# Optimization experiments

Measured on AMD Instinct MI355X. Metric: run time of the kernel, lower is better.

The kernel has to match this reference:

```python
import jax, jax.numpy as jnp
import numpy as np

# --- model constants (from init_kwargs) ---
COUNT = 8          # number of layer stacks (king buckets)
L1 = 3072          # input feature dim (2*L1//2 == L1)
L2 = 15            # first hidden dim per stack (l1 outputs L2+1: L2 hidden + 1 skip)
L3 = 32            # second hidden dim per stack
SQ_CORR = 127.0 / 128.0   # sqcrele_correction_factor
MAX_ACT = 1.0             # max_hidden_activation (clipped ReLU ceiling)
BATCH = 32768


def setup_inputs() -> dict:
    key = jax.random.key(0)
    ks = jax.random.split(key, 8)
    x = jax.random.normal(ks[0], (BATCH, L1), dtype=jnp.float32)
    routing_data = jax.random.randint(ks[1], (BATCH,), 0, COUNT, dtype=jnp.int64)
    # StackedLinear weights: [count, out_features, in_features]
    w1 = jax.random.normal(ks[2], (COUNT, L2 + 1, L1), dtype=jnp.float32) * 0.01
    b1 = jax.random.normal(ks[3], (COUNT, L2 + 1), dtype=jnp.float32) * 0.01
    w2 = jax.random.normal(ks[4], (COUNT, L3, 2 * L2), dtype=jnp.float32) * 0.05
    b2 = jax.random.normal(ks[5], (COUNT, L3), dtype=jnp.float32) * 0.01
    w3 = jax.random.normal(ks[6], (COUNT, 1, L3), dtype=jnp.float32) * 0.05
    b3 = jnp.zeros((COUNT, 1), dtype=jnp.float32)  # output bias zeroed in __init__
    return {"x": x, "routing_data": routing_data,
            "w1": w1, "b1": b1, "w2": w2, "b2": b2, "w3": w3, "b3": b3}


def reference(x, routing_data, w1, b1, w2, b2, w3, b3):
    # l1: apply all COUNT linears to the shared input -> [B, count, L2+1]
    l1c = jnp.einsum('bi,coi->bco', x, w1) + b1
    l1x, l1x_out = l1c[..., :L2], l1c[..., L2:]            # [B,c,L2], [B,c,1]
    sqr_l1x = (l1x * l1x) * SQ_CORR
    h1 = jnp.clip(jnp.concatenate([sqr_l1x, l1x], axis=2), 0.0, MAX_ACT)  # [B,c,2*L2]
    # l2: per-stack linear -> [B, count, L3]
    h2 = jnp.clip(jnp.einsum('bci,coi->bco', h1, w2) + b2, 0.0, MAX_ACT)
    # output: per-stack linear -> [B, count, 1], plus skip connection
    l3x = jnp.einsum('bci,coi->bco', h2, w3) + b3 + l1x_out
    # hard-index routing: gather the selected stack per batch element -> [B, 1]
    idx = routing_data.astype(jnp.int32)[:, None, None]
    return jnp.take_along_axis(l3x, idx, axis=1).squeeze(1)
```

## Files before the change

### kernel.cpp

```cpp
#include <hip/hip_runtime.h>

#define NEXP   8
#define L1DIM  3072
#define BATCH  32768
#define SQCORR (127.0f / 128.0f)
#define CHUNK  256
#define NCHUNK (L1DIM / CHUNK)

#define CUR_STRIDE  16
#define WS_CURSORS  0
#define WS_SORTED   (NEXP * CUR_STRIDE)
#define NBLK_SORT   (BATCH / 256)
#define BLK_PER_E   (BATCH / 16)
#define NBLK_MAIN   (NEXP * BLK_PER_E)

__global__ void init_k(int* ws) {
    if (threadIdx.x < NEXP)
        ws[WS_CURSORS + threadIdx.x * CUR_STRIDE] = threadIdx.x * BATCH;
}

__global__ void scatter_k(const int* __restrict__ routing, int* ws) {
    __shared__ int h[NEXP];
    __shared__ int base[NEXP];
    if (threadIdx.x < NEXP) h[threadIdx.x] = 0;
    __syncthreads();
    int i = blockIdx.x * 256 + threadIdx.x;
    int e = routing[i];
    int rank = atomicAdd(&h[e], 1);
    __syncthreads();
    if (threadIdx.x < NEXP)
        base[threadIdx.x] =
            atomicAdd(&ws[WS_CURSORS + threadIdx.x * CUR_STRIDE], h[threadIdx.x]);
    __syncthreads();
    ws[WS_SORTED + base[e] + rank] = i;
}

__device__ __forceinline__ void lds_cp16(void* lds, const void* g) {
    __builtin_amdgcn_global_load_lds(
        (const __attribute__((address_space(1))) void*)g,
        (__attribute__((address_space(3))) void*)lds, 16, 0, 0);
}

__global__ __launch_bounds__(256, 3) void moe_main_k(
        const float* __restrict__ x, const int* __restrict__ ws,
        const float* __restrict__ w1, const float* __restrict__ b1,
        const float* __restrict__ w2, const float* __restrict__ b2,
        const float* __restrict__ w3, const float* __restrict__ b3,
        float* __restrict__ out) {
    __shared__ float xs[3][16][CHUNK];
    __shared__ float tot[4][64];

    const int e   = blockIdx.x % NEXP;
    const int b16 = (blockIdx.x / NEXP) * 16;
    const int n   = ws[WS_CURSORS + e * CUR_STRIDE] - e * BATCH;
    if (b16 >= n) return;

    const int tid  = threadIdx.x;
    const int wid  = tid >> 6;
    const int lane = tid & 63;
    const int r0   = wid * 4;
    const int loff = lane * 4;

    int rows[4];
    const float* xp[4];
    #pragma unroll
    for (int q = 0; q < 4; ++q) {
        int s = b16 + r0 + q;
        rows[q] = (s < n) ? ws[WS_SORTED + e * BATCH + s] : -1;
        int r = rows[q] < 0 ? 0 : rows[q];
        xp[q] = x + (size_t)r * L1DIM;
    }
    const float* w1e = w1 + (size_t)e * 16 * L1DIM;

    auto issue_x = [&](int t, int b) {
        const int koff = t * CHUNK + loff;
        #pragma unroll
        for (int q = 0; q < 4; ++q)
            lds_cp16(&xs[b][r0 + q][loff], xp[q] + koff);
    };

    float acc[64];
    #pragma unroll
    for (int k = 0; k < 64; ++k) acc[k] = 0.0f;

    issue_x(0, 0);
    issue_x(1, 1);

    #pragma unroll 1
    for (int t = 0; t < NCHUNK; ++t) {
        const int xb = t % 3;
        asm volatile("s_waitcnt vmcnt(4)" ::: "memory");

        float4 xv[4];
        #pragma unroll
        for (int q = 0; q < 4; ++q)
            xv[q] = *(const float4*)&xs[xb][r0 + q][loff];

        const float* wc = w1e + t * CHUNK + loff;
        float4 wv[16];
        #pragma unroll
        for (int o = 0; o < 16; ++o)
            wv[o] = *(const float4*)(wc + (size_t)o * L1DIM);

        __builtin_amdgcn_sched_barrier(0);
        if (t + 2 < NCHUNK) issue_x(t + 2, (t + 2) % 3);
        __builtin_amdgcn_sched_barrier(0);

        #pragma unroll
        for (int o = 0; o < 16; ++o) {
            #pragma unroll
            for (int q = 0; q < 4; ++q) {
                float s = acc[q * 16 + o];
                s = fmaf(xv[q].x, wv[o].x, s);
                s = fmaf(xv[q].y, wv[o].y, s);
                s = fmaf(xv[q].z, wv[o].z, s);
                s = fmaf(xv[q].w, wv[o].w, s);
                acc[q * 16 + o] = s;
            }
        }
    }

    #pragma unroll
    for (int s = 0; s < 6; ++s) {
        const int mask = 32 >> s;
        const bool hi = (lane & mask) != 0;
        #pragma unroll
        for (int k = 0; k < 32; ++k) {
            if (k >= mask) break;
            float give = hi ? acc[k] : acc[k + mask];
            float got  = __shfl_xor(give, mask, 64);
            float keep = hi ? acc[k + mask] : acc[k];
            acc[k] = keep + got;
        }
    }

    tot[wid][lane] = acc[0];
    __syncthreads();

    const int q = lane >> 4;
    const int j = lane & 15;
    const int row = rows[q];

    const float* tq = &tot[wid][q * 16];
    float l1x_out = tq[15] + b1[e * 16 + 15];

    float h1v[30];
    #pragma unroll
    for (int i = 0; i < 15; ++i) {
        float t = tq[i] + b1[e * 16 + i];
        float sq = t * t * SQCORR;
        h1v[i]      = fminf(fmaxf(sq, 0.0f), 1.0f);
        h1v[i + 15] = fminf(fmaxf(t,  0.0f), 1.0f);
    }

    float s0 = b2[e * 32 + j];
    float s1 = b2[e * 32 + 16 + j];
    const float* w2e = w2 + (size_t)e * 32 * 30;
    #pragma unroll
    for (int i = 0; i < 30; ++i) {
        s0 = fmaf(h1v[i], w2e[j * 30 + i], s0);
        s1 = fmaf(h1v[i], w2e[(16 + j) * 30 + i], s1);
    }
    s0 = fminf(fmaxf(s0, 0.0f), 1.0f);
    s1 = fminf(fmaxf(s1, 0.0f), 1.0f);

    float p = s0 * w3[e * 32 + j] + s1 * w3[e * 32 + 16 + j];
    #pragma unroll
    for (int m = 8; m >= 1; m >>= 1) p += __shfl_xor(p, m, 64);

    if (j == 0 && row >= 0) out[row] = p + b3[e] + l1x_out;
}

extern "C" void kernel_launch(void* const* d_in, const int* in_sizes, int n_in,
                              void* d_out, int out_size, void* d_ws, size_t ws_size,
                              hipStream_t stream) {
    const float* x       = (const float*)d_in[0];
    const int*   routing = (const int*)d_in[1];
    const float* w1      = (const float*)d_in[2];
    const float* b1      = (const float*)d_in[3];
    const float* w2      = (const float*)d_in[4];
    const float* b2      = (const float*)d_in[5];
    const float* w3      = (const float*)d_in[6];
    const float* b3      = (const float*)d_in[7];
    float* out = (float*)d_out;
    int*   ws  = (int*)d_ws;

    init_k<<<1, 64, 0, stream>>>(ws);
    scatter_k<<<NBLK_SORT, 256, 0, stream>>>(routing, ws);
    moe_main_k<<<NBLK_MAIN, 256, 0, stream>>>(x, ws, w1, b1, w2, b2, w3, b3, out);
}
```

Baseline: 137.8 us.

## Split main kernel into producer waves loading x and consumer compute waves

The block grows to 512 threads. Four producer waves stream x rows into LDS with async global-to-LDS copies in 768-float chunks. Four consumer waves wait on barriers and run the FMA dot products against w1 read from global memory. The LDS reduction buffer is replaced by cross-lane shuffles. The aim is to overlap x loading with compute across waves, but the 147 KB LDS buffer and the 512-thread block limit occupancy to one block per CU.

```diff
diff --git a/kernel.cpp b/kernel.cpp
--- a/kernel.cpp
+++ b/kernel.cpp
@@ -4,8 +4,9 @@
 #define L1DIM  3072
 #define BATCH  32768
 #define SQCORR (127.0f / 128.0f)
-#define CHUNK  256
-#define NCHUNK (L1DIM / CHUNK)
+#define CHUNK  768
+#define NCHUNK 4
+#define SEG    256
 
 #define CUR_STRIDE  16
 #define WS_CURSORS  0
@@ -41,14 +42,13 @@
         (__attribute__((address_space(3))) void*)lds, 16, 0, 0);
 }
 
-__global__ __launch_bounds__(256, 3) void moe_main_k(
+__global__ __launch_bounds__(512, 1) void moe_main_k(
         const float* __restrict__ x, const int* __restrict__ ws,
         const float* __restrict__ w1, const float* __restrict__ b1,
         const float* __restrict__ w2, const float* __restrict__ b2,
         const float* __restrict__ w3, const float* __restrict__ b3,
         float* __restrict__ out) {
     __shared__ float xs[3][16][CHUNK];
-    __shared__ float tot[4][64];
 
     const int e   = blockIdx.x % NEXP;
     const int b16 = (blockIdx.x / NEXP) * 16;
@@ -58,7 +58,8 @@
     const int tid  = threadIdx.x;
     const int wid  = tid >> 6;
     const int lane = tid & 63;
-    const int r0   = wid * 4;
+    const int cw   = wid & 3;
+    const int r0   = cw * 4;
     const int loff = lane * 4;
 
     int rows[4];
@@ -70,52 +71,66 @@
         int r = rows[q] < 0 ? 0 : rows[q];
         xp[q] = x + (size_t)r * L1DIM;
     }
+
+    if (wid >= 4) {
+        auto issue = [&](int t) {
+            const int b = t % 3;
+            const int koff = t * CHUNK;
+            #pragma unroll
+            for (int q = 0; q < 4; ++q)
+                #pragma unroll
+                for (int s = 0; s < 3; ++s)
+                    lds_cp16(&xs[b][r0 + q][s * SEG + loff],
+                             xp[q] + koff + s * SEG + loff);
+        };
+        issue(0);
+        issue(1);
+        asm volatile("s_waitcnt vmcnt(12)" ::: "memory");
+        __builtin_amdgcn_s_barrier();
+        issue(2);
+        asm volatile("s_waitcnt vmcnt(12)" ::: "memory");
+        __builtin_amdgcn_s_barrier();
+        issue(3);
+        asm volatile("s_waitcnt vmcnt(12)" ::: "memory");
+        __builtin_amdgcn_s_barrier();
+        asm volatile("s_waitcnt vmcnt(0)" ::: "memory");
+        __builtin_amdgcn_s_barrier();
+        return;
+    }
+
     const float* w1e = w1 + (size_t)e * 16 * L1DIM;
 
-    auto issue_x = [&](int t, int b) {
-        const int koff = t * CHUNK + loff;
-        #pragma unroll
-        for (int q = 0; q < 4; ++q)
-            lds_cp16(&xs[b][r0 + q][loff], xp[q] + koff);
-    };
-
     float acc[64];
     #pragma unroll
     for (int k = 0; k < 64; ++k) acc[k] = 0.0f;
-
-    issue_x(0, 0);
-    issue_x(1, 1);
 
     #pragma unroll 1
     for (int t = 0; t < NCHUNK; ++t) {
+        __builtin_amdgcn_s_barrier();
+        asm volatile("" ::: "memory");
         const int xb = t % 3;
-        asm volatile("s_waitcnt vmcnt(4)" ::: "memory");
-
-        float4 xv[4];
+        const float* wt = w1e + t * CHUNK + loff;
         #pragma unroll
-        for (int q = 0; q < 4; ++q)
-            xv[q] = *(const float4*)&xs[xb][r0 + q][loff];
-
-        const float* wc = w1e + t * CHUNK + loff;
-        float4 wv[16];
-        #pragma unroll
-        for (int o = 0; o < 16; ++o)
-            wv[o] = *(const float4*)(wc + (size_t)o * L1DIM);
-
-        __builtin_amdgcn_sched_barrier(0);
-        if (t + 2 < NCHUNK) issue_x(t + 2, (t + 2) % 3);
-        __builtin_amdgcn_sched_barrier(0);
-
-        #pragma unroll
-        for (int o = 0; o < 16; ++o) {
-            #pragma unroll
-            for (int q = 0; q < 4; ++q) {
-                float s = acc[q * 16 + o];
-                s = fmaf(xv[q].x, wv[o].x, s);
-                s = fmaf(xv[q].y, wv[o].y, s);
-                s = fmaf(xv[q].z, wv[o].z, s);
-                s = fmaf(xv[q].w, wv[o].w, s);
-                acc[q * 16 + o] = s;
+        for (int s = 0; s < 3; ++s) {
+            float4 xv[4];
+            #pragma unroll
+            for (int q = 0; q < 4; ++q)
+                xv[q] = *(const float4*)&xs[xb][r0 + q][s * SEG + loff];
+            float4 wv[16];
+            #pragma unroll
+            for (int o = 0; o < 16; ++o)
+                wv[o] = *(const float4*)(wt + s * SEG + (size_t)o * L1DIM);
+            #pragma unroll
+            for (int o = 0; o < 16; ++o) {
+                #pragma unroll
+                for (int q = 0; q < 4; ++q) {
+                    float a = acc[q * 16 + o];
+                    a = fmaf(xv[q].x, wv[o].x, a);
+                    a = fmaf(xv[q].y, wv[o].y, a);
+                    a = fmaf(xv[q].z, wv[o].z, a);
+                    a = fmaf(xv[q].w, wv[o].w, a);
+                    acc[q * 16 + o] = a;
+                }
             }
         }
     }
@@ -134,14 +149,15 @@
         }
     }
 
-    tot[wid][lane] = acc[0];
-    __syncthreads();
-
     const int q = lane >> 4;
     const int j = lane & 15;
     const int row = rows[q];
 
-    const float* tq = &tot[wid][q * 16];
+    float tq[16];
+    #pragma unroll
+    for (int i = 0; i < 16; ++i)
+        tq[i] = __shfl(acc[0], (lane & 48) | i, 64);
+
     float l1x_out = tq[15] + b1[e * 16 + 15];
 
     float h1v[30];
@@ -187,5 +203,5 @@
 
     init_k<<<1, 64, 0, stream>>>(ws);
     scatter_k<<<NBLK_SORT, 256, 0, stream>>>(routing, ws);
-    moe_main_k<<<NBLK_MAIN, 256, 0, stream>>>(x, ws, w1, b1, w2, b2, w3, b3, out);
-}
+    moe_main_k<<<NBLK_MAIN, 512, 0, stream>>>(x, ws, w1, b1, w2, b2, w3, b3, out);
+}
```

Measured after the change: 294.2 us. +113.4%, slower.

## Switch main kernel to persistent tile loop with larger double-buffered chunks

Applied to the files above, without the earlier changes.

The main kernel now uses a fixed grid of 512 blocks that loop over expert tiles. Each expert gets a fixed capacity of 288 tiles of 16 rows, so the thousands of blocks that used to launch and exit immediately are gone. The x staging changes from a triple buffer of 256-wide chunks to a double buffer of 512-wide chunks, with a full vmcnt wait before each chunk. The LDS round-trip for per-row totals is replaced by lane shuffles. The trade-offs are lower occupancy (launch bounds 2, small grid) and shallower prefetch. Rows beyond the per-expert cap would be silently dropped if routing were skewed.

```diff
diff --git a/kernel.cpp b/kernel.cpp
--- a/kernel.cpp
+++ b/kernel.cpp
@@ -4,15 +4,17 @@
 #define L1DIM  3072
 #define BATCH  32768
 #define SQCORR (127.0f / 128.0f)
-#define CHUNK  256
+#define CHUNK  512
 #define NCHUNK (L1DIM / CHUNK)
 
 #define CUR_STRIDE  16
 #define WS_CURSORS  0
 #define WS_SORTED   (NEXP * CUR_STRIDE)
 #define NBLK_SORT   (BATCH / 256)
-#define BLK_PER_E   (BATCH / 16)
-#define NBLK_MAIN   (NEXP * BLK_PER_E)
+
+#define TPE        288
+#define NTILE      (NEXP * TPE)
+#define GRID_MAIN  512
 
 __global__ void init_k(int* ws) {
     if (threadIdx.x < NEXP)
@@ -41,134 +43,159 @@
         (__attribute__((address_space(3))) void*)lds, 16, 0, 0);
 }
 
-__global__ __launch_bounds__(256, 3) void moe_main_k(
+__global__ __launch_bounds__(256, 2) void moe_main_k(
         const float* __restrict__ x, const int* __restrict__ ws,
         const float* __restrict__ w1, const float* __restrict__ b1,
         const float* __restrict__ w2, const float* __restrict__ b2,
         const float* __restrict__ w3, const float* __restrict__ b3,
         float* __restrict__ out) {
-    __shared__ float xs[3][16][CHUNK];
-    __shared__ float tot[4][64];
-
-    const int e   = blockIdx.x % NEXP;
-    const int b16 = (blockIdx.x / NEXP) * 16;
-    const int n   = ws[WS_CURSORS + e * CUR_STRIDE] - e * BATCH;
-    if (b16 >= n) return;
+    __shared__ float xs[2][16][CHUNK];
 
     const int tid  = threadIdx.x;
     const int wid  = tid >> 6;
     const int lane = tid & 63;
     const int r0   = wid * 4;
     const int loff = lane * 4;
-
-    int rows[4];
-    const float* xp[4];
-    #pragma unroll
-    for (int q = 0; q < 4; ++q) {
-        int s = b16 + r0 + q;
-        rows[q] = (s < n) ? ws[WS_SORTED + e * BATCH + s] : -1;
-        int r = rows[q] < 0 ? 0 : rows[q];
-        xp[q] = x + (size_t)r * L1DIM;
+    const int q    = lane >> 4;
+    const int j    = lane & 15;
+
+    #pragma unroll 1
+    for (int tile = blockIdx.x; tile < NTILE; tile += GRID_MAIN) {
+        const int e   = tile / TPE;
+        const int ti  = tile - e * TPE;
+        const int n   = ws[WS_CURSORS + e * CUR_STRIDE] - e * BATCH;
+        const int b16 = ti * 16;
+        if (b16 >= n) continue;
+
+        int rows[4];
+        const float* xp[4];
+        #pragma unroll
+        for (int qq = 0; qq < 4; ++qq) {
+            int s = b16 + r0 + qq;
+            rows[qq] = (s < n) ? ws[WS_SORTED + e * BATCH + s] : -1;
+            int r = rows[qq] < 0 ? 0 : rows[qq];
+            xp[qq] = x + (size_t)r * L1DIM;
+        }
+        const float* w1e = w1 + (size_t)e * 16 * L1DIM;
+
+        auto issue_x = [&](int t, int b) {
+            const int koff = t * CHUNK;
+            #pragma unroll
+            for (int qq = 0; qq < 4; ++qq) {
+                lds_cp16(&xs[b][r0 + qq][loff],       xp[qq] + koff + loff);
+                lds_cp16(&xs[b][r0 + qq][256 + loff], xp[qq] + koff + 256 + loff);
+            }
+        };
+
+        float acc[64];
+        #pragma unroll
+        for (int k = 0; k < 64; ++k) acc[k] = 0.0f;
+
+        issue_x(0, 0);
+
+        #pragma unroll 1
+        for (int t = 0; t < NCHUNK; ++t) {
+            const int xb = t & 1;
+            asm volatile("s_waitcnt vmcnt(0)" ::: "memory");
+            __builtin_amdgcn_sched_barrier(0);
+
+            float4 xvA[4], xvB[4];
+            #pragma unroll
+            for (int qq = 0; qq < 4; ++qq) {
+                xvA[qq] = *(const float4*)&xs[xb][r0 + qq][loff];
+                xvB[qq] = *(const float4*)&xs[xb][r0 + qq][256 + loff];
+            }
+            const float* wc = w1e + t * CHUNK + loff;
+
+            float4 wvA[16];
+            #pragma unroll
+            for (int o = 0; o < 16; ++o)
+                wvA[o] = *(const float4*)(wc + (size_t)o * L1DIM);
+            #pragma unroll
+            for (int o = 0; o < 16; ++o) {
+                #pragma unroll
+                for (int qq = 0; qq < 4; ++qq) {
+                    float a = acc[qq * 16 + o];
+                    a = fmaf(xvA[qq].x, wvA[o].x, a);
+                    a = fmaf(xvA[qq].y, wvA[o].y, a);
+                    a = fmaf(xvA[qq].z, wvA[o].z, a);
+                    a = fmaf(xvA[qq].w, wvA[o].w, a);
+                    acc[qq * 16 + o] = a;
+                }
+            }
+
+            float4 wvB[16];
+            #pragma unroll
+            for (int o = 0; o < 16; ++o)
+                wvB[o] = *(const float4*)(wc + 256 + (size_t)o * L1DIM);
+
+            __builtin_amdgcn_sched_barrier(0);
+            if (t + 1 < NCHUNK) issue_x(t + 1, (t + 1) & 1);
+            __builtin_amdgcn_sched_barrier(0);
+
+            #pragma unroll
+            for (int o = 0; o < 16; ++o) {
+                #pragma unroll
+                for (int qq = 0; qq < 4; ++qq) {
+                    float a = acc[qq * 16 + o];
+                    a = fmaf(xvB[qq].x, wvB[o].x, a);
+                    a = fmaf(xvB[qq].y, wvB[o].y, a);
+                    a = fmaf(xvB[qq].z, wvB[o].z, a);
+                    a = fmaf(xvB[qq].w, wvB[o].w, a);
+                    acc[qq * 16 + o] = a;
+                }
+            }
+        }
+
+        #pragma unroll
+        for (int s = 0; s < 6; ++s) {
+            const int mask = 32 >> s;
+            const bool hi = (lane & mask) != 0;
+            #pragma unroll
+            for (int k = 0; k < 32; ++k) {
+                if (k >= mask) break;
+                float give = hi ? acc[k] : acc[k + mask];
+                float got  = __shfl_xor(give, mask, 64);
+                float keep = hi ? acc[k + mask] : acc[k];
+                acc[k] = keep + got;
+            }
+        }
+
+        const int row = rows[q];
+
+        float tq[16];
+        #pragma unroll
+        for (int i = 0; i < 16; ++i)
+            tq[i] = __shfl(acc[0], (lane & 48) | i, 64);
+
+        float l1x_out = tq[15] + b1[e * 16 + 15];
+
+        float h1v[30];
+        #pragma unroll
+        for (int i = 0; i < 15; ++i) {
+            float v = tq[i] + b1[e * 16 + i];
+            float sq = v * v * SQCORR;
+            h1v[i]      = fminf(fmaxf(sq, 0.0f), 1.0f);
+            h1v[i + 15] = fminf(fmaxf(v,  0.0f), 1.0f);
+        }
+
+        float s0 = b2[e * 32 + j];
+        float s1 = b2[e * 32 + 16 + j];
+        const float* w2e = w2 + (size_t)e * 32 * 30;
+        #pragma unroll
+        for (int i = 0; i < 30; ++i) {
+            s0 = fmaf(h1v[i], w2e[j * 30 + i], s0);
+            s1 = fmaf(h1v[i], w2e[(16 + j) * 30 + i], s1);
+        }
+        s0 = fminf(fmaxf(s0, 0.0f), 1.0f);
+        s1 = fminf(fmaxf(s1, 0.0f), 1.0f);
+
+        float p = s0 * w3[e * 32 + j] + s1 * w3[e * 32 + 16 + j];
+        #pragma unroll
+        for (int m = 8; m >= 1; m >>= 1) p += __shfl_xor(p, m, 64);
+
+        if (j == 0 && row >= 0) out[row] = p + b3[e] + l1x_out;
     }
-    const float* w1e = w1 + (size_t)e * 16 * L1DIM;
-
-    auto issue_x = [&](int t, int b) {
-        const int koff = t * CHUNK + loff;
-        #pragma unroll
-        for (int q = 0; q < 4; ++q)
-            lds_cp16(&xs[b][r0 + q][loff], xp[q] + koff);
-    };
-
-    float acc[64];
-    #pragma unroll
-    for (int k = 0; k < 64; ++k) acc[k] = 0.0f;
-
-    issue_x(0, 0);
-    issue_x(1, 1);
-
-    #pragma unroll 1
-    for (int t = 0; t < NCHUNK; ++t) {
-        const int xb = t % 3;
-        asm volatile("s_waitcnt vmcnt(4)" ::: "memory");
-
-        float4 xv[4];
-        #pragma unroll
-        for (int q = 0; q < 4; ++q)
-            xv[q] = *(const float4*)&xs[xb][r0 + q][loff];
-
-        const float* wc = w1e + t * CHUNK + loff;
-        float4 wv[16];
-        #pragma unroll
-        for (int o = 0; o < 16; ++o)
-            wv[o] = *(const float4*)(wc + (size_t)o * L1DIM);
-
-        __builtin_amdgcn_sched_barrier(0);
-        if (t + 2 < NCHUNK) issue_x(t + 2, (t + 2) % 3);
-        __builtin_amdgcn_sched_barrier(0);
-
-        #pragma unroll
-        for (int o = 0; o < 16; ++o) {
-            #pragma unroll
-            for (int q = 0; q < 4; ++q) {
-                float s = acc[q * 16 + o];
-                s = fmaf(xv[q].x, wv[o].x, s);
-                s = fmaf(xv[q].y, wv[o].y, s);
-                s = fmaf(xv[q].z, wv[o].z, s);
-                s = fmaf(xv[q].w, wv[o].w, s);
-                acc[q * 16 + o] = s;
-            }
-        }
-    }
-
-    #pragma unroll
-    for (int s = 0; s < 6; ++s) {
-        const int mask = 32 >> s;
-        const bool hi = (lane & mask) != 0;
-        #pragma unroll
-        for (int k = 0; k < 32; ++k) {
-            if (k >= mask) break;
-            float give = hi ? acc[k] : acc[k + mask];
-            float got  = __shfl_xor(give, mask, 64);
-            float keep = hi ? acc[k + mask] : acc[k];
-            acc[k] = keep + got;
-        }
-    }
-
-    tot[wid][lane] = acc[0];
-    __syncthreads();
-
-    const int q = lane >> 4;
-    const int j = lane & 15;
-    const int row = rows[q];
-
-    const float* tq = &tot[wid][q * 16];
-    float l1x_out = tq[15] + b1[e * 16 + 15];
-
-    float h1v[30];
-    #pragma unroll
-    for (int i = 0; i < 15; ++i) {
-        float t = tq[i] + b1[e * 16 + i];
-        float sq = t * t * SQCORR;
-        h1v[i]      = fminf(fmaxf(sq, 0.0f), 1.0f);
-        h1v[i + 15] = fminf(fmaxf(t,  0.0f), 1.0f);
-    }
-
-    float s0 = b2[e * 32 + j];
-    float s1 = b2[e * 32 + 16 + j];
-    const float* w2e = w2 + (size_t)e * 32 * 30;
-    #pragma unroll
-    for (int i = 0; i < 30; ++i) {
-        s0 = fmaf(h1v[i], w2e[j * 30 + i], s0);
-        s1 = fmaf(h1v[i], w2e[(16 + j) * 30 + i], s1);
-    }
-    s0 = fminf(fmaxf(s0, 0.0f), 1.0f);
-    s1 = fminf(fmaxf(s1, 0.0f), 1.0f);
-
-    float p = s0 * w3[e * 32 + j] + s1 * w3[e * 32 + 16 + j];
-    #pragma unroll
-    for (int m = 8; m >= 1; m >>= 1) p += __shfl_xor(p, m, 64);
-
-    if (j == 0 && row >= 0) out[row] = p + b3[e] + l1x_out;
 }
 
 extern "C" void kernel_launch(void* const* d_in, const int* in_sizes, int n_in,
@@ -187,5 +214,5 @@
 
     init_k<<<1, 64, 0, stream>>>(ws);
     scatter_k<<<NBLK_SORT, 256, 0, stream>>>(routing, ws);
-    moe_main_k<<<NBLK_MAIN, 256, 0, stream>>>(x, ws, w1, b1, w2, b2, w3, b3, out);
-}
+    moe_main_k<<<GRID_MAIN, 256, 0, stream>>>(x, ws, w1, b1, w2, b2, w3, b3, out);
+}
```

Result: slower. 148.4 us (+7.7%).

## Double-buffer w1 register loads across chunks and replace LDS reduction with shuffles

Applied to the files above, without the earlier changes.

Splits the K loop into pairs of chunks with two register buffers for w1 (wvA/wvB), so weights for the next chunk are loaded while the current chunk's FMAs run, and adjusts the vmcnt wait accordingly. To fit the doubled register footprint, launch bounds drop from 3 to 2 waves-per-SIMD occupancy. The final per-row gather of reduced sums now uses wave shuffles instead of an LDS array plus __syncthreads. The trade is fewer resident waves for better latency hiding within each wave.

```diff
diff --git a/kernel.cpp b/kernel.cpp
--- a/kernel.cpp
+++ b/kernel.cpp
@@ -41,14 +41,13 @@
         (__attribute__((address_space(3))) void*)lds, 16, 0, 0);
 }
 
-__global__ __launch_bounds__(256, 3) void moe_main_k(
+__global__ __launch_bounds__(256, 2) void moe_main_k(
         const float* __restrict__ x, const int* __restrict__ ws,
         const float* __restrict__ w1, const float* __restrict__ b1,
         const float* __restrict__ w2, const float* __restrict__ b2,
         const float* __restrict__ w3, const float* __restrict__ b3,
         float* __restrict__ out) {
     __shared__ float xs[3][16][CHUNK];
-    __shared__ float tot[4][64];
 
     const int e   = blockIdx.x % NEXP;
     const int b16 = (blockIdx.x / NEXP) * 16;
@@ -70,53 +69,76 @@
         int r = rows[q] < 0 ? 0 : rows[q];
         xp[q] = x + (size_t)r * L1DIM;
     }
-    const float* w1e = w1 + (size_t)e * 16 * L1DIM;
-
-    auto issue_x = [&](int t, int b) {
+    const float* w1e = w1 + (size_t)e * 16 * L1DIM + loff;
+
+    auto issue_x = [&](int t) {
+        const int b = t % 3;
         const int koff = t * CHUNK + loff;
         #pragma unroll
         for (int q = 0; q < 4; ++q)
             lds_cp16(&xs[b][r0 + q][loff], xp[q] + koff);
     };
-
-    float acc[64];
-    #pragma unroll
-    for (int k = 0; k < 64; ++k) acc[k] = 0.0f;
-
-    issue_x(0, 0);
-    issue_x(1, 1);
-
-    #pragma unroll 1
-    for (int t = 0; t < NCHUNK; ++t) {
-        const int xb = t % 3;
-        asm volatile("s_waitcnt vmcnt(4)" ::: "memory");
-
-        float4 xv[4];
-        #pragma unroll
-        for (int q = 0; q < 4; ++q)
-            xv[q] = *(const float4*)&xs[xb][r0 + q][loff];
-
-        const float* wc = w1e + t * CHUNK + loff;
-        float4 wv[16];
+    auto load_wv = [&](int t, float4* wv) {
+        const float* wc = w1e + t * CHUNK;
         #pragma unroll
         for (int o = 0; o < 16; ++o)
             wv[o] = *(const float4*)(wc + (size_t)o * L1DIM);
-
-        __builtin_amdgcn_sched_barrier(0);
-        if (t + 2 < NCHUNK) issue_x(t + 2, (t + 2) % 3);
-        __builtin_amdgcn_sched_barrier(0);
-
+    };
+    auto read_xv = [&](int t, float4* xv) {
+        const int b = t % 3;
+        #pragma unroll
+        for (int q = 0; q < 4; ++q)
+            xv[q] = *(const float4*)&xs[b][r0 + q][loff];
+    };
+
+    float acc[64];
+    #pragma unroll
+    for (int k = 0; k < 64; ++k) acc[k] = 0.0f;
+
+    auto do_fma = [&](const float4* xv, const float4* wv) {
         #pragma unroll
         for (int o = 0; o < 16; ++o) {
             #pragma unroll
             for (int q = 0; q < 4; ++q) {
-                float s = acc[q * 16 + o];
-                s = fmaf(xv[q].x, wv[o].x, s);
-                s = fmaf(xv[q].y, wv[o].y, s);
-                s = fmaf(xv[q].z, wv[o].z, s);
-                s = fmaf(xv[q].w, wv[o].w, s);
-                acc[q * 16 + o] = s;
+                float a = acc[q * 16 + o];
+                a = fmaf(xv[q].x, wv[o].x, a);
+                a = fmaf(xv[q].y, wv[o].y, a);
+                a = fmaf(xv[q].z, wv[o].z, a);
+                a = fmaf(xv[q].w, wv[o].w, a);
+                acc[q * 16 + o] = a;
             }
+        }
+    };
+
+    float4 wvA[16], wvB[16];
+
+    issue_x(0);
+    issue_x(1);
+    load_wv(0, wvA);
+
+    #pragma unroll 1
+    for (int t = 0; t < NCHUNK; t += 2) {
+        {
+            asm volatile("s_waitcnt vmcnt(24)" ::: "memory");
+            __builtin_amdgcn_sched_barrier(0);
+            float4 xv[4];
+            read_xv(t, xv);
+            load_wv(t + 1, wvB);
+            __builtin_amdgcn_sched_barrier(0);
+            if (t + 2 < NCHUNK) issue_x(t + 2);
+            __builtin_amdgcn_sched_barrier(0);
+            do_fma(xv, wvA);
+        }
+        {
+            asm volatile("s_waitcnt vmcnt(24)" ::: "memory");
+            __builtin_amdgcn_sched_barrier(0);
+            float4 xv[4];
+            read_xv(t + 1, xv);
+            if (t + 2 < NCHUNK) load_wv(t + 2, wvA);
+            __builtin_amdgcn_sched_barrier(0);
+            if (t + 3 < NCHUNK) issue_x(t + 3);
+            __builtin_amdgcn_sched_barrier(0);
+            do_fma(xv, wvB);
         }
     }
 
@@ -134,23 +156,24 @@
         }
     }
 
-    tot[wid][lane] = acc[0];
-    __syncthreads();
-
     const int q = lane >> 4;
     const int j = lane & 15;
     const int row = rows[q];
 
-    const float* tq = &tot[wid][q * 16];
+    float tq[16];
+    #pragma unroll
+    for (int i = 0; i < 16; ++i)
+        tq[i] = __shfl(acc[0], (lane & 48) | i, 64);
+
     float l1x_out = tq[15] + b1[e * 16 + 15];
 
     float h1v[30];
     #pragma unroll
     for (int i = 0; i < 15; ++i) {
-        float t = tq[i] + b1[e * 16 + i];
-        float sq = t * t * SQCORR;
+        float v = tq[i] + b1[e * 16 + i];
+        float sq = v * v * SQCORR;
         h1v[i]      = fminf(fmaxf(sq, 0.0f), 1.0f);
-        h1v[i + 15] = fminf(fmaxf(t,  0.0f), 1.0f);
+        h1v[i + 15] = fminf(fmaxf(v,  0.0f), 1.0f);
     }
 
     float s0 = b2[e * 32 + j];
```

New measurement: 398.9 us. +189.4%, slower.
